# Kernel tuning notes

Measured on AMD Instinct MI355X. Metric: run time of the kernel, lower is better.

The kernel has to match this reference:

```python
import jax, jax.numpy as jnp
import numpy as np

N = 100000      # nodes
E = 1600000     # edges (avg degree 16)
IN_F, HID, OUT_F, NC = 384, 128, 64, 2
EPS = 1e-5
NEG_SLOPE = 0.01


def _layernorm(x, g, b):
    m = jnp.mean(x, axis=-1, keepdims=True)
    v = jnp.var(x, axis=-1, keepdims=True)
    return (x - m) * jax.lax.rsqrt(v + EPS) * g + b


def _graph_conv(x, edge_index, edge_weight, w_rel, b_rel, w_root):
    # PyG GraphConv: lin_rel(scatter_add(w_e * x[src] -> dst)) + lin_root(x)
    src, dst = edge_index[0], edge_index[1]
    msg = x[src] * edge_weight[:, None]                      # [E, C]
    agg = jax.ops.segment_sum(msg, dst, num_segments=x.shape[0])  # [N, C]
    return agg @ w_rel.T + b_rel + x @ w_root.T


def _xavier(key, shape):
    fan_in, fan_out = shape[1], shape[0]
    lim = float(np.sqrt(6.0 / (fan_in + fan_out)))
    return jax.random.uniform(key, shape, jnp.float32, -lim, lim)


def setup_inputs() -> dict:
    key = jax.random.key(0)
    ks = jax.random.split(key, 10)
    x = jax.random.normal(ks[0], (N, IN_F), jnp.float32)
    edge_index = jax.random.randint(ks[1], (2, E), 0, N, jnp.int64)
    edge_attr = jax.random.uniform(ks[2], (E,), jnp.float32)
    return {
        "x": x,
        "edge_index": edge_index,
        "edge_attr": edge_attr,
        "ln1_g": jnp.ones((IN_F,), jnp.float32),
        "ln1_b": jnp.zeros((IN_F,), jnp.float32),
        "fc1_w": _xavier(ks[3], (HID, IN_F)),
        "fc1_b": jnp.zeros((HID,), jnp.float32),
        "c1_wrel": _xavier(ks[4], (HID, HID)),
        "c1_brel": jnp.zeros((HID,), jnp.float32),
        "c1_wroot": _xavier(ks[5], (HID, HID)),
        "c2_wrel": _xavier(ks[6], (OUT_F, HID)),
        "c2_brel": jnp.zeros((OUT_F,), jnp.float32),
        "c2_wroot": _xavier(ks[7], (OUT_F, HID)),
        "ln2_g": jnp.ones((OUT_F,), jnp.float32),
        "ln2_b": jnp.zeros((OUT_F,), jnp.float32),
        "fc2_w": _xavier(ks[8], (NC, OUT_F)),
        "fc2_b": jnp.zeros((NC,), jnp.float32),
    }


def reference(x, edge_index, edge_attr,
              ln1_g, ln1_b, fc1_w, fc1_b,
              c1_wrel, c1_brel, c1_wroot,
              c2_wrel, c2_brel, c2_wroot,
              ln2_g, ln2_b, fc2_w, fc2_b):
    h = _layernorm(x, ln1_g, ln1_b) @ fc1_w.T + fc1_b          # [N, HID]
    h = _graph_conv(h, edge_index, edge_attr, c1_wrel, c1_brel, c1_wroot)
    h = jax.nn.leaky_relu(h, NEG_SLOPE)
    h = _graph_conv(h, edge_index, edge_attr, c2_wrel, c2_brel, c2_wroot)
    h = jax.nn.leaky_relu(h, NEG_SLOPE)                        # [N, OUT_F]
    out = _layernorm(h, ln2_g, ln2_b) @ fc2_w.T + fc2_b        # [N, NC]
    return out
```

## Files before the change

kernel.cpp:

```cpp
#include <hip/hip_runtime.h>
#include <hip/hip_bf16.h>

#define N_IN_F 384
#define N_HID  128
#define N_OUT  64

typedef unsigned short ushort_t;
typedef __attribute__((ext_vector_type(8))) short short8v;
typedef __attribute__((ext_vector_type(4))) float floatx4;

union U8 { uint4 v; unsigned short u[8]; };

__device__ __forceinline__ float bfu2f(unsigned short s){
    union { unsigned i; float f; } c; c.i = ((unsigned)s) << 16; return c.f;
}
__device__ __forceinline__ unsigned short f2bfu(float f){
    __hip_bfloat16 h = __float2bfloat16(f);
    union { __hip_bfloat16 h; unsigned short u; } c; c.h = h; return c.u;
}

__device__ __forceinline__ float loadS(const void* p, size_t i, int fm){
    return fm ? bfu2f(((const unsigned short*)p)[i]) : ((const float*)p)[i];
}

__global__ void k_detect_all(const int* __restrict__ ei, const unsigned* __restrict__ xw,
                             int* __restrict__ modep){
    int lane = threadIdx.x & 63;
    int zi = 0;
    if (lane < 32) zi = ei[2*lane + 1];
    int cnt = 0;
    #pragma unroll
    for (int q = 0; q < 8; q++){
        unsigned w = xw[lane*8 + q];
        unsigned elo = (w >> 7) & 0xff;
        cnt += (elo >= 118 && elo <= 134) ? 1 : 0;
    }
    #pragma unroll
    for (int m = 32; m; m >>= 1){ zi |= __shfl_xor(zi, m, 64); cnt += __shfl_xor(cnt, m, 64); }
    if (lane == 0 && blockIdx.x == 0){
        modep[0] = (zi == 0) ? 1 : 0;
        modep[1] = (cnt >= 256) ? 1 : 0;
    }
}

__device__ __forceinline__ int edge_src(const int* ei, int e, int i, int mode){
    return mode ? ei[2*(size_t)i] : ei[i];
}
__device__ __forceinline__ int edge_dst(const int* ei, int e, int i, int mode){
    return mode ? ei[2*(size_t)e + 2*(size_t)i] : ei[(size_t)e + i];
}

__global__ void k_hist(const int* __restrict__ ei, int e, int n, const int* __restrict__ modep,
                       int* __restrict__ deg){
    int i = blockIdx.x * 256 + threadIdx.x;
    if (i >= e) return;
    int mode = modep[0];
    int d = edge_dst(ei, e, i, mode);
    if ((unsigned)d >= (unsigned)n) return;
    atomicAdd(&deg[d], 1);
}

__global__ __launch_bounds__(1024) void k_blksum(
    const int* __restrict__ deg, int n, int* __restrict__ part)
{
    __shared__ int s[1024];
    int i = blockIdx.x * 1024 + threadIdx.x;
    s[threadIdx.x] = (i < n) ? deg[i] : 0;
    __syncthreads();
    for (int off = 512; off; off >>= 1){
        if (threadIdx.x < off) s[threadIdx.x] += s[threadIdx.x + off];
        __syncthreads();
    }
    if (threadIdx.x == 0) part[blockIdx.x] = s[0];
}

__global__ __launch_bounds__(128) void k_scanpart(
    int* __restrict__ part, int nb, int* __restrict__ rowoff, int n)
{
    __shared__ int s[128];
    int t = threadIdx.x;
    if (nb <= 128){
        int v = (t < nb) ? part[t] : 0;
        s[t] = v; __syncthreads();
        #pragma unroll
        for (int off = 1; off < 128; off <<= 1){
            int tmp = (t >= off) ? s[t - off] : 0;
            __syncthreads();
            s[t] += tmp;
            __syncthreads();
        }
        if (t < nb) part[t] = s[t] - v;
        if (t == 127) rowoff[n] = s[127];
    } else if (t == 0){
        int run = 0;
        for (int b = 0; b < nb; b++){ int tt = part[b]; part[b] = run; run += tt; }
        rowoff[n] = run;
    }
}

__global__ __launch_bounds__(1024) void k_scanblk(
    int* __restrict__ deg, const int* __restrict__ part, int n, int* __restrict__ rowoff)
{
    __shared__ int s[1024];
    int t = threadIdx.x;
    int i = blockIdx.x * 1024 + t;
    int v = (i < n) ? deg[i] : 0;
    s[t] = v; __syncthreads();
    for (int off = 1; off < 1024; off <<= 1){
        int tmp = (t >= off) ? s[t - off] : 0;
        __syncthreads();
        s[t] += tmp;
        __syncthreads();
    }
    if (i < n){
        int excl = s[t] - v + part[blockIdx.x];
        rowoff[i] = excl;
        deg[i]    = excl;
    }
}

__global__ void k_scatter(const int* __restrict__ ei, const void* __restrict__ ea,
                          int e, int n, const int* __restrict__ modep,
                          int* __restrict__ cursor, int* __restrict__ col,
                          float* __restrict__ wgt)
{
    int i = blockIdx.x * 256 + threadIdx.x;
    if (i >= e) return;
    int mode = modep[0], fm = modep[1];
    int d = edge_dst(ei, e, i, mode);
    if ((unsigned)d >= (unsigned)n) return;
    int s = edge_src(ei, e, i, mode);
    if ((unsigned)s >= (unsigned)n) s = 0;
    int pos = atomicAdd(&cursor[d], 1);
    if ((unsigned)pos >= (unsigned)e) return;
    col[pos] = s;
    wgt[pos] = loadS(ea, i, fm);
}

__global__ __launch_bounds__(64) void k_prep_w1(
    const void* __restrict__ W, const void* __restrict__ g, const void* __restrict__ b,
    const void* __restrict__ fc1b, const int* __restrict__ fmp,
    ushort_t* __restrict__ Wp, float* __restrict__ u, float* __restrict__ v)
{
    int fm = fmp[0];
    int j = blockIdx.x, lane = threadIdx.x;
    float su = 0.f, sv = 0.f;
    for (int k = lane; k < N_IN_F; k += 64){
        float w  = loadS(W, (size_t)j*N_IN_F + k, fm);
        float gk = loadS(g, k, fm);
        float bk = loadS(b, k, fm);
        unsigned short pw = f2bfu(gk * w);
        Wp[(size_t)j*N_IN_F + k] = pw;
        su += bfu2f(pw);
        sv += bk * w;
    }
    #pragma unroll
    for (int m = 32; m; m >>= 1){ su += __shfl_xor(su, m, 64); sv += __shfl_xor(sv, m, 64); }
    if (lane == 0){
        u[j] = su;
        v[j] = sv + loadS(fc1b, j, fm);
    }
}

__global__ void k_cvt4(const void* __restrict__ p0, const void* __restrict__ p1,
                       const void* __restrict__ p2, const void* __restrict__ p3,
                       const int* __restrict__ fmp, ushort_t* __restrict__ o)
{
    int fm = fmp[0];
    int i = blockIdx.x * 256 + threadIdx.x;
    if (i >= 49152) return;
    const void* p; int off;
    if (i < 16384)      { p = p0; off = i; }
    else if (i < 32768) { p = p1; off = i - 16384; }
    else if (i < 40960) { p = p2; off = i - 32768; }
    else                { p = p3; off = i - 40960; }
    o[i] = f2bfu(loadS(p, off, fm));
}

__global__ __launch_bounds__(256) void k_gemm1_mfma(
    const void* __restrict__ x, const int* __restrict__ fmp,
    const ushort_t* __restrict__ Wp,
    const float* __restrict__ u, const float* __restrict__ v,
    ushort_t* __restrict__ out, int n)
{
    int fm = fmp[0];
    int t = threadIdx.x;
    int wave = t >> 6, lane = t & 63;
    int r16 = lane & 15, kq = lane >> 4;
    int m0 = blockIdx.x * 128 + wave * 32;

    int rA[2];
    rA[0] = min(m0 + r16,      n - 1);
    rA[1] = min(m0 + 16 + r16, n - 1);

    floatx4 acc[2][8];
    #pragma unroll
    for (int a = 0; a < 2; a++)
        #pragma unroll
        for (int c = 0; c < 8; c++)
            acc[a][c] = (floatx4){0.f, 0.f, 0.f, 0.f};

    float s1[2] = {0.f, 0.f}, s2[2] = {0.f, 0.f};

    for (int ks = 0; ks < N_IN_F/32; ks++){
        int kb = ks*32 + kq*8;
        short8v af[2];
        #pragma unroll
        for (int mi = 0; mi < 2; mi++){
            size_t idx = (size_t)rA[mi]*N_IN_F + kb;
            float f[8];
            if (fm){
                short8v sv = *(const short8v*)((const ushort_t*)x + idx);
                af[mi] = sv;
                #pragma unroll
                for (int q = 0; q < 8; q++) f[q] = bfu2f((unsigned short)sv[q]);
            } else {
                const float* xf = (const float*)x + idx;
                floatx4 p = *(const floatx4*)xf;
                floatx4 q4 = *(const floatx4*)(xf + 4);
                f[0]=p[0]; f[1]=p[1]; f[2]=p[2]; f[3]=p[3];
                f[4]=q4[0]; f[5]=q4[1]; f[6]=q4[2]; f[7]=q4[3];
                short8v r;
                #pragma unroll
                for (int q = 0; q < 8; q++) r[q] = (short)f2bfu(f[q]);
                af[mi] = r;
            }
            #pragma unroll
            for (int q = 0; q < 8; q++){ s1[mi] += f[q]; s2[mi] += f[q]*f[q]; }
        }
        short8v bfr[8];
        #pragma unroll
        for (int ni = 0; ni < 8; ni++)
            bfr[ni] = *(const short8v*)(Wp + (size_t)(ni*16 + r16)*N_IN_F + kb);
        #pragma unroll
        for (int mi = 0; mi < 2; mi++)
            #pragma unroll
            for (int ni = 0; ni < 8; ni++)
                acc[mi][ni] = __builtin_amdgcn_mfma_f32_16x16x32_bf16(
                    af[mi], bfr[ni], acc[mi][ni], 0, 0, 0);
    }

    float mu[2], rs[2];
    #pragma unroll
    for (int mi = 0; mi < 2; mi++){
        s1[mi] += __shfl_xor(s1[mi], 16, 64); s1[mi] += __shfl_xor(s1[mi], 32, 64);
        s2[mi] += __shfl_xor(s2[mi], 16, 64); s2[mi] += __shfl_xor(s2[mi], 32, 64);
        mu[mi] = s1[mi] * (1.f/384.f);
        float var = fmaxf(s2[mi] * (1.f/384.f) - mu[mi]*mu[mi], 0.f);
        rs[mi] = rsqrtf(var + 1e-5f);
    }

    #pragma unroll
    for (int mi = 0; mi < 2; mi++){
        int ib = m0 + mi*16 + kq*4;
        float mm[4], rr[4];
        #pragma unroll
        for (int r = 0; r < 4; r++){
            mm[r] = __shfl(mu[mi], kq*4 + r, 64);
            rr[r] = __shfl(rs[mi], kq*4 + r, 64);
        }
        #pragma unroll
        for (int ni = 0; ni < 8; ni++){
            int j = ni*16 + r16;
            float uj = u[j], vj = v[j];
            #pragma unroll
            for (int r = 0; r < 4; r++){
                int ii = ib + r;
                float val = rr[r]*acc[mi][ni][r] - rr[r]*mm[r]*uj + vj;
                if (ii < n) out[(size_t)ii*N_HID + j] = f2bfu(val);
            }
        }
    }
}

template<int BN>
__global__ __launch_bounds__(256) void k_conv_mfma(
    const ushort_t* __restrict__ A1, const ushort_t* __restrict__ A2,
    const ushort_t* __restrict__ W1, const ushort_t* __restrict__ W2,
    const void* __restrict__ bias, const int* __restrict__ fmp,
    ushort_t* __restrict__ out, int n)
{
    constexpr int NT = BN / 16;
    int fm = fmp[0];
    int t = threadIdx.x;
    int wave = t >> 6, lane = t & 63;
    int r16 = lane & 15, kq = lane >> 4;
    int m0 = blockIdx.x * 128 + wave * 32;

    int rA[2];
    rA[0] = min(m0 + r16,      n - 1);
    rA[1] = min(m0 + 16 + r16, n - 1);

    floatx4 acc[2][NT];
    #pragma unroll
    for (int a = 0; a < 2; a++)
        #pragma unroll
        for (int c = 0; c < NT; c++)
            acc[a][c] = (floatx4){0.f, 0.f, 0.f, 0.f};

    #pragma unroll
    for (int p = 0; p < 2; p++){
        const ushort_t* A = p ? A2 : A1;
        const ushort_t* W = p ? W2 : W1;
        #pragma unroll
        for (int ks = 0; ks < 4; ks++){
            int kb = ks*32 + kq*8;
            short8v af[2], bfr[NT];
            #pragma unroll
            for (int mi = 0; mi < 2; mi++)
                af[mi] = *(const short8v*)(A + (size_t)rA[mi]*N_HID + kb);
            #pragma unroll
            for (int ni = 0; ni < NT; ni++)
                bfr[ni] = *(const short8v*)(W + (size_t)(ni*16 + r16)*N_HID + kb);
            #pragma unroll
            for (int mi = 0; mi < 2; mi++)
                #pragma unroll
                for (int ni = 0; ni < NT; ni++)
                    acc[mi][ni] = __builtin_amdgcn_mfma_f32_16x16x32_bf16(
                        af[mi], bfr[ni], acc[mi][ni], 0, 0, 0);
        }
    }

    #pragma unroll
    for (int ni = 0; ni < NT; ni++){
        int j = ni*16 + r16;
        float bb = loadS(bias, j, fm);
        #pragma unroll
        for (int mi = 0; mi < 2; mi++){
            int ib = m0 + mi*16 + kq*4;
            #pragma unroll
            for (int r = 0; r < 4; r++){
                int ii = ib + r;
                float val = acc[mi][ni][r] + bb;
                val = (val >= 0.f) ? val : 0.01f * val;
                if (ii < n) out[(size_t)ii*BN + j] = f2bfu(val);
            }
        }
    }
}

__global__ __launch_bounds__(256) void k_agg(
    const int* __restrict__ rowoff, const int* __restrict__ col,
    const float* __restrict__ wgt,
    const ushort_t* __restrict__ src_mat,
    ushort_t* __restrict__ out, int n, int eTot)
{
    int t = threadIdx.x;
    int lane = t & 63;
    int d = blockIdx.x * 4 + (t >> 6);
    if (d >= n) return;
    int grp = lane >> 4;
    int c16 = lane & 15;
    int e0 = rowoff[d], e1 = rowoff[d+1];
    e0 = max(0, min(e0, eTot));
    e1 = max(e0, min(e1, eTot));
    float acc[8] = {};
    for (int e = e0 + grp; e < e1; e += 4){
        int s = col[e];
        if ((unsigned)s >= (unsigned)n) s = 0;
        float wv = wgt[e];
        U8 u; u.v = *(const uint4*)(src_mat + (size_t)s*N_HID + c16*8);
        #pragma unroll
        for (int q = 0; q < 8; q++) acc[q] += wv * bfu2f(u.u[q]);
    }
    #pragma unroll
    for (int q = 0; q < 8; q++){
        acc[q] += __shfl_xor(acc[q], 16, 64);
        acc[q] += __shfl_xor(acc[q], 32, 64);
    }
    if (grp == 0){
        union { ushort_t u[8]; uint4 v; } P;
        #pragma unroll
        for (int q = 0; q < 8; q++) P.u[q] = f2bfu(acc[q]);
        *(uint4*)(out + (size_t)d*N_HID + c16*8) = P.v;
    }
}

__global__ __launch_bounds__(256) void k_final(
    const ushort_t* __restrict__ g2,
    const void* __restrict__ gam, const void* __restrict__ bet,
    const void* __restrict__ W, const void* __restrict__ bias,
    const int* __restrict__ fmp,
    void* __restrict__ out, int n)
{
    int fm   = fmp[0];
    int lane = threadIdx.x & 63;
    int i    = blockIdx.x * 4 + (threadIdx.x >> 6);
    if (i >= n) return;
    float z = bfu2f(g2[(size_t)i*64 + lane]);
    float s = z, s2 = z*z;
    #pragma unroll
    for (int m = 32; m; m >>= 1){ s += __shfl_xor(s, m, 64); s2 += __shfl_xor(s2, m, 64); }
    float mu   = s * (1.f/64.f);
    float var  = fmaxf(s2 * (1.f/64.f) - mu*mu, 0.f);
    float rstd = rsqrtf(var + 1e-5f);
    float zn = (z - mu) * rstd * loadS(gam, lane, fm) + loadS(bet, lane, fm);
    float p0 = zn * loadS(W, lane, fm);
    float p1 = zn * loadS(W, 64 + lane, fm);
    #pragma unroll
    for (int m = 32; m; m >>= 1){ p0 += __shfl_xor(p0, m, 64); p1 += __shfl_xor(p1, m, 64); }
    if (lane == 0){
        float o0 = p0 + loadS(bias, 0, fm);
        float o1 = p1 + loadS(bias, 1, fm);
        if (fm){
            ushort_t* ob = (ushort_t*)out;
            ob[(size_t)i*2]     = f2bfu(o0);
            ob[(size_t)i*2 + 1] = f2bfu(o1);
        } else {
            float* of = (float*)out;
            of[(size_t)i*2]     = o0;
            of[(size_t)i*2 + 1] = o1;
        }
    }
}

extern "C" void kernel_launch(void* const* d_in, const int* in_sizes, int n_in,
                              void* d_out, int out_size, void* d_ws, size_t ws_size,
                              hipStream_t stream)
{
    const void* x     = d_in[0];
    const int*  ei    = (const int*)d_in[1];
    const void* ea    = d_in[2];
    const void* ln1g  = d_in[3];
    const void* ln1b  = d_in[4];
    const void* fc1w  = d_in[5];
    const void* fc1b  = d_in[6];
    const void* c1rel = d_in[7];
    const void* c1bre = d_in[8];
    const void* c1roo = d_in[9];
    const void* c2rel = d_in[10];
    const void* c2bre = d_in[11];
    const void* c2roo = d_in[12];
    const void* ln2g  = d_in[13];
    const void* ln2b  = d_in[14];
    const void* fc2w  = d_in[15];
    const void* fc2b  = d_in[16];
    (void)n_in; (void)out_size; (void)ws_size;

    const int n = in_sizes[0] / N_IN_F;
    const int e = in_sizes[2];

    char* wsp = (char*)d_ws;
    size_t off = 0;
    auto alloc = [&](size_t bytes) -> char* {
        char* p = wsp + off; off += (bytes + 255) & ~(size_t)255; return p;
    };
    int*      deg    = (int*)  alloc((size_t)n * 4);
    int*      rowoff = (int*)  alloc((size_t)(n+1) * 4);
    int*      part   = (int*)  alloc(4096);
    int*      modep  = (int*)  alloc(256);
    int*      col    = (int*)  alloc((size_t)e * 4);
    float*    wgt    = (float*)alloc((size_t)e * 4);
    float*    u      = (float*)alloc(128 * 4);
    float*    v      = (float*)alloc(128 * 4);
    ushort_t* Wp     = (ushort_t*)alloc((size_t)N_HID * N_IN_F * 2);
    ushort_t* cw     = (ushort_t*)alloc((size_t)49152 * 2);
    ushort_t* h1     = (ushort_t*)alloc((size_t)n * N_HID * 2);
    ushort_t* agg1   = (ushort_t*)alloc((size_t)n * N_HID * 2);
    ushort_t* g1     = (ushort_t*)alloc((size_t)n * N_HID * 2);
    ushort_t* agg2   = h1;
    ushort_t* g2     = agg1;

    hipMemsetAsync(deg, 0, (size_t)n * 4, stream);
    k_detect_all<<<1, 64, 0, stream>>>(ei, (const unsigned*)x, modep);

    int nb = (n + 1023) / 1024;
    k_hist    <<<(e + 255) / 256, 256, 0, stream>>>(ei, e, n, modep, deg);
    k_blksum  <<<nb, 1024, 0, stream>>>(deg, n, part);
    k_scanpart<<<1, 128, 0, stream>>>(part, nb, rowoff, n);
    k_scanblk <<<nb, 1024, 0, stream>>>(deg, part, n, rowoff);
    k_scatter <<<(e + 255) / 256, 256, 0, stream>>>(ei, ea, e, n, modep, deg, col, wgt);

    k_prep_w1<<<N_HID, 64, 0, stream>>>(fc1w, ln1g, ln1b, fc1b, modep + 1, Wp, u, v);
    k_cvt4   <<<(49152 + 255) / 256, 256, 0, stream>>>(c1rel, c1roo, c2rel, c2roo, modep + 1, cw);

    k_gemm1_mfma<<<(n + 127) / 128, 256, 0, stream>>>(x, modep + 1, Wp, u, v, h1, n);

    k_agg<<<(n + 3) / 4, 256, 0, stream>>>(rowoff, col, wgt, h1, agg1, n, e);
    k_conv_mfma<128><<<(n + 127) / 128, 256, 0, stream>>>(agg1, h1, cw, cw + 16384, c1bre, modep + 1, g1, n);

    k_agg<<<(n + 3) / 4, 256, 0, stream>>>(rowoff, col, wgt, g1, agg2, n, e);
    k_conv_mfma<64><<<(n + 127) / 128, 256, 0, stream>>>(agg2, g1, cw + 32768, cw + 40960, c2bre, modep + 1, g2, n);

    k_final<<<(n + 3) / 4, 256, 0, stream>>>(g2, ln2g, ln2b, fc2w, fc2b, modep + 1, d_out, n);
}
```

Before: 728.3 us.

## Fuse final layernorm+fc into conv2, pack CSR col/weight, shrink GEMM row tiles

Three changes. The final LayerNorm and 2-class linear head are fused into the second graph-conv MFMA kernel, so the g2 intermediate is no longer written and read back and one launch goes away. CSR column indices and edge weights are packed into one int2 array, so the aggregation kernels do one 8-byte load per edge instead of two separate loads. All MFMA GEMM kernels drop from 32 rows per wave to 16, which doubles the grid and lowers register use per wave but reloads the weight fragments for each 16 rows.

```diff
diff --git a/kernel.cpp b/kernel.cpp
--- a/kernel.cpp
+++ b/kernel.cpp
@@ -121,8 +121,7 @@
 
 __global__ void k_scatter(const int* __restrict__ ei, const void* __restrict__ ea,
                           int e, int n, const int* __restrict__ modep,
-                          int* __restrict__ cursor, int* __restrict__ col,
-                          float* __restrict__ wgt)
+                          int* __restrict__ cursor, int2* __restrict__ colw)
 {
     int i = blockIdx.x * 256 + threadIdx.x;
     if (i >= e) return;
@@ -133,8 +132,8 @@
     if ((unsigned)s >= (unsigned)n) s = 0;
     int pos = atomicAdd(&cursor[d], 1);
     if ((unsigned)pos >= (unsigned)e) return;
-    col[pos] = s;
-    wgt[pos] = loadS(ea, i, fm);
+    int2 pk; pk.x = s; pk.y = __float_as_int(loadS(ea, i, fm));
+    colw[pos] = pk;
 }
 
 __global__ __launch_bounds__(64) void k_prep_w1(
@@ -187,116 +186,89 @@
     int t = threadIdx.x;
     int wave = t >> 6, lane = t & 63;
     int r16 = lane & 15, kq = lane >> 4;
-    int m0 = blockIdx.x * 128 + wave * 32;
-
-    int rA[2];
-    rA[0] = min(m0 + r16,      n - 1);
-    rA[1] = min(m0 + 16 + r16, n - 1);
-
-    floatx4 acc[2][8];
-    #pragma unroll
-    for (int a = 0; a < 2; a++)
-        #pragma unroll
-        for (int c = 0; c < 8; c++)
-            acc[a][c] = (floatx4){0.f, 0.f, 0.f, 0.f};
-
-    float s1[2] = {0.f, 0.f}, s2[2] = {0.f, 0.f};
+    int m0 = blockIdx.x * 64 + wave * 16;
+    int rA = min(m0 + r16, n - 1);
+
+    floatx4 acc[8];
+    #pragma unroll
+    for (int c = 0; c < 8; c++) acc[c] = (floatx4){0.f, 0.f, 0.f, 0.f};
+    float s1 = 0.f, s2 = 0.f;
 
     for (int ks = 0; ks < N_IN_F/32; ks++){
         int kb = ks*32 + kq*8;
-        short8v af[2];
-        #pragma unroll
-        for (int mi = 0; mi < 2; mi++){
-            size_t idx = (size_t)rA[mi]*N_IN_F + kb;
-            float f[8];
-            if (fm){
-                short8v sv = *(const short8v*)((const ushort_t*)x + idx);
-                af[mi] = sv;
-                #pragma unroll
-                for (int q = 0; q < 8; q++) f[q] = bfu2f((unsigned short)sv[q]);
-            } else {
-                const float* xf = (const float*)x + idx;
-                floatx4 p = *(const floatx4*)xf;
-                floatx4 q4 = *(const floatx4*)(xf + 4);
-                f[0]=p[0]; f[1]=p[1]; f[2]=p[2]; f[3]=p[3];
-                f[4]=q4[0]; f[5]=q4[1]; f[6]=q4[2]; f[7]=q4[3];
-                short8v r;
-                #pragma unroll
-                for (int q = 0; q < 8; q++) r[q] = (short)f2bfu(f[q]);
-                af[mi] = r;
-            }
+        size_t idx = (size_t)rA*N_IN_F + kb;
+        short8v af;
+        float f[8];
+        if (fm){
+            short8v sv = *(const short8v*)((const ushort_t*)x + idx);
+            af = sv;
             #pragma unroll
-            for (int q = 0; q < 8; q++){ s1[mi] += f[q]; s2[mi] += f[q]*f[q]; }
-        }
+            for (int q = 0; q < 8; q++) f[q] = bfu2f((unsigned short)sv[q]);
+        } else {
+            const float* xf = (const float*)x + idx;
+            floatx4 p = *(const floatx4*)xf;
+            floatx4 q4 = *(const floatx4*)(xf + 4);
+            f[0]=p[0]; f[1]=p[1]; f[2]=p[2]; f[3]=p[3];
+            f[4]=q4[0]; f[5]=q4[1]; f[6]=q4[2]; f[7]=q4[3];
+            short8v r;
+            #pragma unroll
+            for (int q = 0; q < 8; q++) r[q] = (short)f2bfu(f[q]);
+            af = r;
+        }
+        #pragma unroll
+        for (int q = 0; q < 8; q++){ s1 += f[q]; s2 += f[q]*f[q]; }
+
         short8v bfr[8];
         #pragma unroll
         for (int ni = 0; ni < 8; ni++)
             bfr[ni] = *(const short8v*)(Wp + (size_t)(ni*16 + r16)*N_IN_F + kb);
         #pragma unroll
-        for (int mi = 0; mi < 2; mi++)
-            #pragma unroll
-            for (int ni = 0; ni < 8; ni++)
-                acc[mi][ni] = __builtin_amdgcn_mfma_f32_16x16x32_bf16(
-                    af[mi], bfr[ni], acc[mi][ni], 0, 0, 0);
-    }
-
-    float mu[2], rs[2];
-    #pragma unroll
-    for (int mi = 0; mi < 2; mi++){
-        s1[mi] += __shfl_xor(s1[mi], 16, 64); s1[mi] += __shfl_xor(s1[mi], 32, 64);
-        s2[mi] += __shfl_xor(s2[mi], 16, 64); s2[mi] += __shfl_xor(s2[mi], 32, 64);
-        mu[mi] = s1[mi] * (1.f/384.f);
-        float var = fmaxf(s2[mi] * (1.f/384.f) - mu[mi]*mu[mi], 0.f);
-        rs[mi] = rsqrtf(var + 1e-5f);
-    }
-
-    #pragma unroll
-    for (int mi = 0; mi < 2; mi++){
-        int ib = m0 + mi*16 + kq*4;
-        float mm[4], rr[4];
-        #pragma unroll
-        for (int r = 0; r < 4; r++){
-            mm[r] = __shfl(mu[mi], kq*4 + r, 64);
-            rr[r] = __shfl(rs[mi], kq*4 + r, 64);
-        }
-        #pragma unroll
-        for (int ni = 0; ni < 8; ni++){
-            int j = ni*16 + r16;
-            float uj = u[j], vj = v[j];
-            #pragma unroll
-            for (int r = 0; r < 4; r++){
-                int ii = ib + r;
-                float val = rr[r]*acc[mi][ni][r] - rr[r]*mm[r]*uj + vj;
-                if (ii < n) out[(size_t)ii*N_HID + j] = f2bfu(val);
-            }
-        }
-    }
-}
-
-template<int BN>
-__global__ __launch_bounds__(256) void k_conv_mfma(
+        for (int ni = 0; ni < 8; ni++)
+            acc[ni] = __builtin_amdgcn_mfma_f32_16x16x32_bf16(af, bfr[ni], acc[ni], 0, 0, 0);
+    }
+
+    s1 += __shfl_xor(s1, 16, 64); s1 += __shfl_xor(s1, 32, 64);
+    s2 += __shfl_xor(s2, 16, 64); s2 += __shfl_xor(s2, 32, 64);
+    float mu = s1 * (1.f/384.f);
+    float var = fmaxf(s2 * (1.f/384.f) - mu*mu, 0.f);
+    float rs = rsqrtf(var + 1e-5f);
+
+    int ib = m0 + kq*4;
+    float mm[4], rr[4];
+    #pragma unroll
+    for (int r = 0; r < 4; r++){
+        mm[r] = __shfl(mu, kq*4 + r, 64);
+        rr[r] = __shfl(rs, kq*4 + r, 64);
+    }
+    #pragma unroll
+    for (int ni = 0; ni < 8; ni++){
+        int j = ni*16 + r16;
+        float uj = u[j], vj = v[j];
+        #pragma unroll
+        for (int r = 0; r < 4; r++){
+            int ii = ib + r;
+            float val = rr[r]*acc[ni][r] - rr[r]*mm[r]*uj + vj;
+            if (ii < n) out[(size_t)ii*N_HID + j] = f2bfu(val);
+        }
+    }
+}
+
+__global__ __launch_bounds__(256) void k_conv1_mfma(
     const ushort_t* __restrict__ A1, const ushort_t* __restrict__ A2,
     const ushort_t* __restrict__ W1, const ushort_t* __restrict__ W2,
     const void* __restrict__ bias, const int* __restrict__ fmp,
     ushort_t* __restrict__ out, int n)
 {
-    constexpr int NT = BN / 16;
     int fm = fmp[0];
     int t = threadIdx.x;
     int wave = t >> 6, lane = t & 63;
     int r16 = lane & 15, kq = lane >> 4;
-    int m0 = blockIdx.x * 128 + wave * 32;
-
-    int rA[2];
-    rA[0] = min(m0 + r16,      n - 1);
-    rA[1] = min(m0 + 16 + r16, n - 1);
-
-    floatx4 acc[2][NT];
-    #pragma unroll
-    for (int a = 0; a < 2; a++)
-        #pragma unroll
-        for (int c = 0; c < NT; c++)
-            acc[a][c] = (floatx4){0.f, 0.f, 0.f, 0.f};
+    int m0 = blockIdx.x * 64 + wave * 16;
+    int rA = min(m0 + r16, n - 1);
+
+    floatx4 acc[8];
+    #pragma unroll
+    for (int c = 0; c < 8; c++) acc[c] = (floatx4){0.f, 0.f, 0.f, 0.f};
 
     #pragma unroll
     for (int p = 0; p < 2; p++){
@@ -305,43 +277,138 @@
         #pragma unroll
         for (int ks = 0; ks < 4; ks++){
             int kb = ks*32 + kq*8;
-            short8v af[2], bfr[NT];
+            short8v af = *(const short8v*)(A + (size_t)rA*N_HID + kb);
+            short8v bfr[8];
             #pragma unroll
-            for (int mi = 0; mi < 2; mi++)
-                af[mi] = *(const short8v*)(A + (size_t)rA[mi]*N_HID + kb);
-            #pragma unroll
-            for (int ni = 0; ni < NT; ni++)
+            for (int ni = 0; ni < 8; ni++)
                 bfr[ni] = *(const short8v*)(W + (size_t)(ni*16 + r16)*N_HID + kb);
             #pragma unroll
-            for (int mi = 0; mi < 2; mi++)
-                #pragma unroll
-                for (int ni = 0; ni < NT; ni++)
-                    acc[mi][ni] = __builtin_amdgcn_mfma_f32_16x16x32_bf16(
-                        af[mi], bfr[ni], acc[mi][ni], 0, 0, 0);
-        }
-    }
-
-    #pragma unroll
-    for (int ni = 0; ni < NT; ni++){
+            for (int ni = 0; ni < 8; ni++)
+                acc[ni] = __builtin_amdgcn_mfma_f32_16x16x32_bf16(af, bfr[ni], acc[ni], 0, 0, 0);
+        }
+    }
+
+    int ib = m0 + kq*4;
+    #pragma unroll
+    for (int ni = 0; ni < 8; ni++){
         int j = ni*16 + r16;
         float bb = loadS(bias, j, fm);
         #pragma unroll
-        for (int mi = 0; mi < 2; mi++){
-            int ib = m0 + mi*16 + kq*4;
+        for (int r = 0; r < 4; r++){
+            int ii = ib + r;
+            float val = acc[ni][r] + bb;
+            val = (val >= 0.f) ? val : 0.01f * val;
+            if (ii < n) out[(size_t)ii*N_HID + j] = f2bfu(val);
+        }
+    }
+}
+
+__global__ __launch_bounds__(256) void k_conv2_final(
+    const ushort_t* __restrict__ A1, const ushort_t* __restrict__ A2,
+    const ushort_t* __restrict__ W1, const ushort_t* __restrict__ W2,
+    const void* __restrict__ bias,
+    const void* __restrict__ gam, const void* __restrict__ bet,
+    const void* __restrict__ Wfc, const void* __restrict__ bfc,
+    const int* __restrict__ fmp, void* __restrict__ out, int n)
+{
+    int fm = fmp[0];
+    int t = threadIdx.x;
+    int wave = t >> 6, lane = t & 63;
+    int r16 = lane & 15, kq = lane >> 4;
+    int m0 = blockIdx.x * 64 + wave * 16;
+    int rA = min(m0 + r16, n - 1);
+
+    floatx4 acc[4];
+    #pragma unroll
+    for (int c = 0; c < 4; c++) acc[c] = (floatx4){0.f, 0.f, 0.f, 0.f};
+
+    #pragma unroll
+    for (int p = 0; p < 2; p++){
+        const ushort_t* A = p ? A2 : A1;
+        const ushort_t* W = p ? W2 : W1;
+        #pragma unroll
+        for (int ks = 0; ks < 4; ks++){
+            int kb = ks*32 + kq*8;
+            short8v af = *(const short8v*)(A + (size_t)rA*N_HID + kb);
+            short8v bfr[4];
             #pragma unroll
-            for (int r = 0; r < 4; r++){
-                int ii = ib + r;
-                float val = acc[mi][ni][r] + bb;
-                val = (val >= 0.f) ? val : 0.01f * val;
-                if (ii < n) out[(size_t)ii*BN + j] = f2bfu(val);
+            for (int ni = 0; ni < 4; ni++)
+                bfr[ni] = *(const short8v*)(W + (size_t)(ni*16 + r16)*N_HID + kb);
+            #pragma unroll
+            for (int ni = 0; ni < 4; ni++)
+                acc[ni] = __builtin_amdgcn_mfma_f32_16x16x32_bf16(af, bfr[ni], acc[ni], 0, 0, 0);
+        }
+    }
+
+    float s[4] = {}, s2[4] = {};
+    #pragma unroll
+    for (int ni = 0; ni < 4; ni++){
+        int j = ni*16 + r16;
+        float bb = loadS(bias, j, fm);
+        #pragma unroll
+        for (int r = 0; r < 4; r++){
+            float val = acc[ni][r] + bb;
+            val = (val >= 0.f) ? val : 0.01f * val;
+            acc[ni][r] = val;
+            s[r] += val; s2[r] += val*val;
+        }
+    }
+    #pragma unroll
+    for (int m = 1; m < 16; m <<= 1){
+        #pragma unroll
+        for (int r = 0; r < 4; r++){
+            s[r]  += __shfl_xor(s[r],  m, 64);
+            s2[r] += __shfl_xor(s2[r], m, 64);
+        }
+    }
+    float mu[4], rstd[4];
+    #pragma unroll
+    for (int r = 0; r < 4; r++){
+        mu[r] = s[r] * (1.f/64.f);
+        float var = fmaxf(s2[r] * (1.f/64.f) - mu[r]*mu[r], 0.f);
+        rstd[r] = rsqrtf(var + 1e-5f);
+    }
+    float p0[4] = {}, p1[4] = {};
+    #pragma unroll
+    for (int ni = 0; ni < 4; ni++){
+        int j = ni*16 + r16;
+        float gj = loadS(gam, j, fm), bj = loadS(bet, j, fm);
+        float w0 = loadS(Wfc, j, fm), w1 = loadS(Wfc, 64 + j, fm);
+        #pragma unroll
+        for (int r = 0; r < 4; r++){
+            float zn = (acc[ni][r] - mu[r]) * rstd[r] * gj + bj;
+            p0[r] += zn * w0;
+            p1[r] += zn * w1;
+        }
+    }
+    #pragma unroll
+    for (int m = 1; m < 16; m <<= 1){
+        #pragma unroll
+        for (int r = 0; r < 4; r++){
+            p0[r] += __shfl_xor(p0[r], m, 64);
+            p1[r] += __shfl_xor(p1[r], m, 64);
+        }
+    }
+    if (r16 == 0){
+        float b0 = loadS(bfc, 0, fm), b1 = loadS(bfc, 1, fm);
+        #pragma unroll
+        for (int r = 0; r < 4; r++){
+            int ii = m0 + kq*4 + r;
+            if (ii >= n) continue;
+            float o0 = p0[r] + b0, o1 = p1[r] + b1;
+            if (fm){
+                unsigned pk = ((unsigned)f2bfu(o1) << 16) | (unsigned)f2bfu(o0);
+                *(unsigned*)((ushort_t*)out + (size_t)ii*2) = pk;
+            } else {
+                float2 f2; f2.x = o0; f2.y = o1;
+                *(float2*)((float*)out + (size_t)ii*2) = f2;
             }
         }
     }
 }
 
 __global__ __launch_bounds__(256) void k_agg(
-    const int* __restrict__ rowoff, const int* __restrict__ col,
-    const float* __restrict__ wgt,
+    const int* __restrict__ rowoff, const int2* __restrict__ colw,
     const ushort_t* __restrict__ src_mat,
     ushort_t* __restrict__ out, int n, int eTot)
 {
@@ -356,9 +423,10 @@
     e1 = max(e0, min(e1, eTot));
     float acc[8] = {};
     for (int e = e0 + grp; e < e1; e += 4){
-        int s = col[e];
+        int2 cw = colw[e];
+        int s = cw.x;
         if ((unsigned)s >= (unsigned)n) s = 0;
-        float wv = wgt[e];
+        float wv = __int_as_float(cw.y);
         U8 u; u.v = *(const uint4*)(src_mat + (size_t)s*N_HID + c16*8);
         #pragma unroll
         for (int q = 0; q < 8; q++) acc[q] += wv * bfu2f(u.u[q]);
@@ -373,44 +441,6 @@
         #pragma unroll
         for (int q = 0; q < 8; q++) P.u[q] = f2bfu(acc[q]);
         *(uint4*)(out + (size_t)d*N_HID + c16*8) = P.v;
-    }
-}
-
-__global__ __launch_bounds__(256) void k_final(
-    const ushort_t* __restrict__ g2,
-    const void* __restrict__ gam, const void* __restrict__ bet,
-    const void* __restrict__ W, const void* __restrict__ bias,
-    const int* __restrict__ fmp,
-    void* __restrict__ out, int n)
-{
-    int fm   = fmp[0];
-    int lane = threadIdx.x & 63;
-    int i    = blockIdx.x * 4 + (threadIdx.x >> 6);
-    if (i >= n) return;
-    float z = bfu2f(g2[(size_t)i*64 + lane]);
-    float s = z, s2 = z*z;
-    #pragma unroll
-    for (int m = 32; m; m >>= 1){ s += __shfl_xor(s, m, 64); s2 += __shfl_xor(s2, m, 64); }
-    float mu   = s * (1.f/64.f);
-    float var  = fmaxf(s2 * (1.f/64.f) - mu*mu, 0.f);
-    float rstd = rsqrtf(var + 1e-5f);
-    float zn = (z - mu) * rstd * loadS(gam, lane, fm) + loadS(bet, lane, fm);
-    float p0 = zn * loadS(W, lane, fm);
-    float p1 = zn * loadS(W, 64 + lane, fm);
-    #pragma unroll
-    for (int m = 32; m; m >>= 1){ p0 += __shfl_xor(p0, m, 64); p1 += __shfl_xor(p1, m, 64); }
-    if (lane == 0){
-        float o0 = p0 + loadS(bias, 0, fm);
-        float o1 = p1 + loadS(bias, 1, fm);
-        if (fm){
-            ushort_t* ob = (ushort_t*)out;
-            ob[(size_t)i*2]     = f2bfu(o0);
-            ob[(size_t)i*2 + 1] = f2bfu(o1);
-        } else {
-            float* of = (float*)out;
-            of[(size_t)i*2]     = o0;
-            of[(size_t)i*2 + 1] = o1;
-        }
     }
 }
 
@@ -449,8 +479,7 @@
     int*      rowoff = (int*)  alloc((size_t)(n+1) * 4);
     int*      part   = (int*)  alloc(4096);
     int*      modep  = (int*)  alloc(256);
-    int*      col    = (int*)  alloc((size_t)e * 4);
-    float*    wgt    = (float*)alloc((size_t)e * 4);
+    int2*     colw   = (int2*) alloc((size_t)e * 8);
     float*    u      = (float*)alloc(128 * 4);
     float*    v      = (float*)alloc(128 * 4);
     ushort_t* Wp     = (ushort_t*)alloc((size_t)N_HID * N_IN_F * 2);
@@ -459,7 +488,6 @@
     ushort_t* agg1   = (ushort_t*)alloc((size_t)n * N_HID * 2);
     ushort_t* g1     = (ushort_t*)alloc((size_t)n * N_HID * 2);
     ushort_t* agg2   = h1;
-    ushort_t* g2     = agg1;
 
     hipMemsetAsync(deg, 0, (size_t)n * 4, stream);
     k_detect_all<<<1, 64, 0, stream>>>(ei, (const unsigned*)x, modep);
@@ -469,18 +497,17 @@
     k_blksum  <<<nb, 1024, 0, stream>>>(deg, n, part);
     k_scanpart<<<1, 128, 0, stream>>>(part, nb, rowoff, n);
     k_scanblk <<<nb, 1024, 0, stream>>>(deg, part, n, rowoff);
-    k_scatter <<<(e + 255) / 256, 256, 0, stream>>>(ei, ea, e, n, modep, deg, col, wgt);
+    k_scatter <<<(e + 255) / 256, 256, 0, stream>>>(ei, ea, e, n, modep, deg, colw);
 
     k_prep_w1<<<N_HID, 64, 0, stream>>>(fc1w, ln1g, ln1b, fc1b, modep + 1, Wp, u, v);
     k_cvt4   <<<(49152 + 255) / 256, 256, 0, stream>>>(c1rel, c1roo, c2rel, c2roo, modep + 1, cw);
 
-    k_gemm1_mfma<<<(n + 127) / 128, 256, 0, stream>>>(x, modep + 1, Wp, u, v, h1, n);
-
-    k_agg<<<(n + 3) / 4, 256, 0, stream>>>(rowoff, col, wgt, h1, agg1, n, e);
-    k_conv_mfma<128><<<(n + 127) / 128, 256, 0, stream>>>(agg1, h1, cw, cw + 16384, c1bre, modep + 1, g1, n);
-
-    k_agg<<<(n + 3) / 4, 256, 0, stream>>>(rowoff, col, wgt, g1, agg2, n, e);
-    k_conv_mfma<64><<<(n + 127) / 128, 256, 0, stream>>>(agg2, g1, cw + 32768, cw + 40960, c2bre, modep + 1, g2, n);
-
-    k_final<<<(n + 3) / 4, 256, 0, stream>>>(g2, ln2g, ln2b, fc2w, fc2b, modep + 1, d_out, n);
-}
+    k_gemm1_mfma<<<(n + 63) / 64, 256, 0, stream>>>(x, modep + 1, Wp, u, v, h1, n);
+
+    k_agg<<<(n + 3) / 4, 256, 0, stream>>>(rowoff, colw, h1, agg1, n, e);
+    k_conv1_mfma<<<(n + 63) / 64, 256, 0, stream>>>(agg1, h1, cw, cw + 16384, c1bre, modep + 1, g1, n);
+
+    k_agg<<<(n + 3) / 4, 256, 0, stream>>>(rowoff, colw, g1, agg2, n, e);
+    k_conv2_final<<<(n + 63) / 64, 256, 0, stream>>>(agg2, g1, cw + 32768, cw + 40960, c2bre,
+                                                     ln2g, ln2b, fc2w, fc2b, modep + 1, d_out, n);
+}
```

After: 754.2 us. 3.6% more time.
